# Performance work log

Measured on AMD Instinct MI355X. Metric: run time of the kernel, lower is better.

The kernel has to match this reference:

```python
import jax, jax.numpy as jnp
import numpy as np

EMBED_DIM = 200
INPUT_DIM = 512


def setup_inputs() -> dict:
    key = jax.random.key(0)
    k1, k2, k3, k4 = jax.random.split(key, 4)
    B, L, T = 64, 256, 64
    x = jax.random.normal(k1, (B, L, INPUT_DIM), dtype=jnp.float32)
    y = jax.random.normal(k2, (B, T, INPUT_DIM), dtype=jnp.float32)
    # fc = nn.Linear(input_dim, embedding_dim)
    W = jax.random.normal(k3, (EMBED_DIM, INPUT_DIM), dtype=jnp.float32) * (1.0 / np.sqrt(INPUT_DIM))
    b = jax.random.normal(k4, (EMBED_DIM,), dtype=jnp.float32) * 0.01
    return {"x": x, "y": y, "W": W, "b": b}


def reference(x, y, W, b):
    # Project both modalities (last dim != embedding_dim in original triggers fc)
    xp = jnp.einsum('bld,ed->ble', x, W) + b   # B x L x E
    yp = jnp.einsum('btd,ed->bte', y, W) + b   # B x T x E
    # Pairwise matchmap: for pair (i, j), matchmap = xp[i] @ yp[j].T -> L x T
    mm = jnp.einsum('ile,jte->ijlt', xp, yp)   # B x B x L x T
    # MISA: max over L (rows of matchmap, dim 0), then mean over T
    S = jnp.max(mm, axis=2).mean(axis=2)       # B x B
    return S
```

## Files before the change

kernel.cpp:

```cpp
#include <hip/hip_runtime.h>
#include <hip/hip_bf16.h>
#include <stdint.h>

#define BB 64
#define LL 256
#define TT 64
#define DD 512
#define EE 200
#define EP 208
#define NKK 13
#define NROWS_X 16384
#define BSTRIDE 264
#define PBM 80

typedef __attribute__((ext_vector_type(8))) short short8;
typedef __attribute__((ext_vector_type(4))) float floatx4;
typedef __attribute__((ext_vector_type(16))) float floatx16;

__device__ __forceinline__ short f2bf(float f) {
  uint32_t u = __builtin_bit_cast(uint32_t, f);
  u = (u + 0x7fffu + ((u >> 16) & 1u)) >> 16;
  return (short)u;
}

__device__ __forceinline__ uint32_t pack2(float lo, float hi) {
  return __builtin_amdgcn_perm(__builtin_bit_cast(uint32_t, hi),
                               __builtin_bit_cast(uint32_t, lo), 0x07060302u);
}

typedef const __attribute__((address_space(1))) uint32_t gu32_t;
typedef __attribute__((address_space(3))) uint32_t lu32_t;
__device__ __forceinline__ void glds16(const void* g, void* l) {
  __builtin_amdgcn_global_load_lds((gu32_t*)g, (lu32_t*)l, 16, 0, 0);
}

#define VMCNT_BARRIER(N) asm volatile("s_waitcnt vmcnt(" #N ") lgkmcnt(0)\n\ts_barrier" ::: "memory")

__global__ void wcvt_kernel(const float* __restrict__ W, short* __restrict__ Wb) {
  const int t = blockIdx.x * 256 + threadIdx.x;
  const int base = t * 8;
  const int e = base >> 9;
  short8 o;
  if (e < EE) {
    const floatx4 f0 = *(const floatx4*)(W + base);
    const floatx4 f1 = *(const floatx4*)(W + base + 4);
    o[0] = f2bf(f0.x); o[1] = f2bf(f0.y); o[2] = f2bf(f0.z); o[3] = f2bf(f0.w);
    o[4] = f2bf(f1.x); o[5] = f2bf(f1.y); o[6] = f2bf(f1.z); o[7] = f2bf(f1.w);
  } else {
    o = (short8)0;
  }
  *(short8*)(Wb + base) = o;
}

__global__ __launch_bounds__(320, 1) void proj_kernel(const float* __restrict__ x,
                                                      const float* __restrict__ y,
                                                      const short* __restrict__ Wb,
                                                      const float* __restrict__ bias,
                                                      short* __restrict__ pT) {
  __shared__ __align__(16) char smem[71680];
  float* ldsA = (float*)smem;
  short* ldsB = (short*)(smem + 30720);
  short* bounce = (short*)smem;

  const int tid  = threadIdx.x;
  const int lane = tid & 63;
  const int wid  = tid >> 6;
  const int r16   = lane & 15;
  const int khalf = lane >> 4;

  const int row0 = blockIdx.x * PBM;

  floatx4 acc[NKK];
#pragma unroll
  for (int n = 0; n < NKK; n++) acc[n] = (floatx4){0.f, 0.f, 0.f, 0.f};

  auto stage = [&](int buf, int ks) {
#pragma unroll
    for (int it = 0; it < 2; it++) {
      const int p = it * 320 + tid;
      const int r = p >> 3, c = p & 7;
      const int gr = row0 + r;
      const float* src = (gr < NROWS_X) ? (x + (size_t)gr * DD)
                                        : (y + (size_t)(gr - NROWS_X) * DD);
      glds16(src + ks * 32 + ((c ^ (r & 7)) << 2),
             &ldsA[buf * 2560 + p * 4]);
    }
#pragma unroll
    for (int it = 0; it < 3; it++) {
      const int p = it * 320 + tid;
      if (it < 2 || tid < 192) {
        const int r = p >> 2, c = p & 3;
        glds16(Wb + (size_t)r * DD + ks * 32 + ((c ^ ((r >> 1) & 3)) << 3),
               &ldsB[buf * 6656 + p * 8]);
      }
    }
  };

  auto compute = [&](int s) {
    const int buf = s % 3;
    const int r = wid * 16 + r16;
    const int c0 = (2 * khalf) ^ (r & 7);
    const int c1 = (2 * khalf + 1) ^ (r & 7);
    const floatx4 f0 = *(const floatx4*)&ldsA[buf * 2560 + r * 32 + c0 * 4];
    const floatx4 f1 = *(const floatx4*)&ldsA[buf * 2560 + r * 32 + c1 * 4];
    union { short8 s8; uint32_t u[4]; } af;
    af.u[0] = pack2(f0.x, f0.y);
    af.u[1] = pack2(f0.z, f0.w);
    af.u[2] = pack2(f1.x, f1.y);
    af.u[3] = pack2(f1.z, f1.w);
    const int bcol = (khalf ^ ((r16 >> 1) & 3)) << 3;
#pragma unroll
    for (int n = 0; n < NKK; n++) {
      const int erow = n * 16 + r16;
      const short8 bfrag = *(const short8*)&ldsB[buf * 6656 + erow * 32 + bcol];
      acc[n] = __builtin_amdgcn_mfma_f32_16x16x32_bf16(af.s8, bfrag, acc[n], 0, 0, 0);
    }
  };

  stage(0, 0);
  stage(1, 1);

  for (int s = 0; s < 15; s++) {
    VMCNT_BARRIER(4);
    if (s + 2 < 16) stage((s + 2) % 3, s + 2);
    compute(s);
  }
  VMCNT_BARRIER(0);
  compute(15);

  __syncthreads();

#pragma unroll
  for (int n = 0; n < NKK; n++) {
    const int e = n * 16 + r16;
    const float bv = (e < EE) ? bias[e] : 0.0f;
#pragma unroll
    for (int rr = 0; rr < 4; rr++) {
      const int lr = wid * 16 + khalf * 4 + rr;
      bounce[lr * BSTRIDE + e] = f2bf(acc[n][rr] + bv);
    }
  }
  __syncthreads();

  for (int c = tid; c < 2080; c += 320) {
    const int n    = c / 160;
    const int rem  = c - n * 160;
    const int lrow = rem >> 1;
    const int eh   = rem & 1;
    const int gr   = row0 + lrow;
    const short8 piece = *(const short8*)&bounce[lrow * BSTRIDE + n * 16 + eh * 8];
    *(short8*)&pT[((size_t)((gr >> 5) * 13 + n)) * 512 + (size_t)(((eh << 5) | (gr & 31)) * 8)] = piece;
  }
}

__global__ __launch_bounds__(512, 2) void pair_kernel(const short* __restrict__ xpT,
                                                      const short* __restrict__ ypT,
                                                      float* __restrict__ S) {
  __shared__ __align__(16) char lds[2 * 53248 + 16384];
  float* red = (float*)(lds + 2 * 53248);

  const int tid  = threadIdx.x;
  const int lane = tid & 63;
  const int wid  = tid >> 6;
  const int jj2  = wid >> 2;
  const int wj   = wid & 3;
  const int bid  = blockIdx.x;
  const int i    = bid & 63;
  const int jq   = bid >> 6;
  const int jbase = jq * 16;

  short8 a0[NKK], a1[NKK];
  {
    const short* ab0 = xpT + ((size_t)((i * 8 + wj * 2 + 0) * NKK)) * 512 + lane * 8;
    const short* ab1 = xpT + ((size_t)((i * 8 + wj * 2 + 1) * NKK)) * 512 + lane * 8;
#pragma unroll
    for (int kk = 0; kk < NKK; kk++) {
      a0[kk] = *(const short8*)(ab0 + kk * 512);
      a1[kk] = *(const short8*)(ab1 + kk * 512);
    }
  }

  auto stageB = [&](int g) {
    const short* src = ypT + (size_t)(jbase + g * 2) * 26 * 512;
    char* dst = lds + (g & 1) * 53248;
    for (int c = tid; c < 3328; c += 512)
      glds16(src + (size_t)c * 8, dst + c * 16);
  };

  stageB(0);
  __syncthreads();

  for (int g = 0; g < 8; g++) {
    if (g + 1 < 8) stageB(g + 1);

    const int j = g * 2 + jj2;
    const short* bbase = (const short*)(lds + (g & 1) * 53248) +
                         (size_t)(jj2 * 26 * 512) + lane * 8;

    floatx16 accA0n0, accA0n1, accA1n0, accA1n1;
#pragma unroll
    for (int r = 0; r < 16; r++) {
      accA0n0[r] = 0.f; accA0n1[r] = 0.f; accA1n0[r] = 0.f; accA1n1[r] = 0.f;
    }

#pragma unroll
    for (int kk = 0; kk < NKK; kk++) {
      const short8 b0 = *(const short8*)(bbase + (0 * NKK + kk) * 512);
      const short8 b1 = *(const short8*)(bbase + (1 * NKK + kk) * 512);
      accA0n0 = __builtin_amdgcn_mfma_f32_32x32x16_bf16(a0[kk], b0, accA0n0, 0, 0, 0);
      accA1n0 = __builtin_amdgcn_mfma_f32_32x32x16_bf16(a1[kk], b0, accA1n0, 0, 0, 0);
      accA0n1 = __builtin_amdgcn_mfma_f32_32x32x16_bf16(a0[kk], b1, accA0n1, 0, 0, 0);
      accA1n1 = __builtin_amdgcn_mfma_f32_32x32x16_bf16(a1[kk], b1, accA1n1, 0, 0, 0);
    }

    float v0 = accA0n0[0], v1 = accA0n1[0];
#pragma unroll
    for (int r = 0; r < 16; r++) {
      v0 = fmaxf(v0, accA0n0[r]); v0 = fmaxf(v0, accA1n0[r]);
      v1 = fmaxf(v1, accA0n1[r]); v1 = fmaxf(v1, accA1n1[r]);
    }
    v0 = fmaxf(v0, __shfl_xor(v0, 32, 64));
    v1 = fmaxf(v1, __shfl_xor(v1, 32, 64));
    if (lane < 32) {
      red[(j * 4 + wj) * 64 + 0 * 32 + lane] = v0;
      red[(j * 4 + wj) * 64 + 1 * 32 + lane] = v1;
    }

    __syncthreads();
  }

#pragma unroll
  for (int rep = 0; rep < 2; rep++) {
    const int j = wid * 2 + rep;
    const int t = lane;
    float v = red[(j * 4 + 0) * 64 + t];
    v = fmaxf(v, red[(j * 4 + 1) * 64 + t]);
    v = fmaxf(v, red[(j * 4 + 2) * 64 + t]);
    v = fmaxf(v, red[(j * 4 + 3) * 64 + t]);
    v += __shfl_xor(v, 1, 64);
    v += __shfl_xor(v, 2, 64);
    v += __shfl_xor(v, 4, 64);
    v += __shfl_xor(v, 8, 64);
    v += __shfl_xor(v, 16, 64);
    v += __shfl_xor(v, 32, 64);
    if (t == 0) S[i * BB + jbase + j] = v * (1.0f / 64.0f);
  }
}

extern "C" void kernel_launch(void* const* d_in, const int* in_sizes, int n_in,
                              void* d_out, int out_size, void* d_ws, size_t ws_size,
                              hipStream_t stream) {
  const float* x = (const float*)d_in[0];
  const float* y = (const float*)d_in[1];
  const float* W = (const float*)d_in[2];
  const float* b = (const float*)d_in[3];
  float* S = (float*)d_out;

  char* ws = (char*)d_ws;
  short* Wb = (short*)ws;
  short* pT = (short*)(ws + 262144);
  short* ypT = pT + (size_t)6656 * 512;

  wcvt_kernel<<<52, 256, 0, stream>>>(W, Wb);
  proj_kernel<<<256, 320, 0, stream>>>(x, y, Wb, b, pT);
  pair_kernel<<<256, 512, 0, stream>>>(pT, ypT, S);
}
```

Before: 45.43 us.

## Split projection N dimension across three wave groups with 960-thread blocks

The projection kernel grows from 5 to 15 waves per block. Each group of 5 waves covers the 16-row M tiles, but only about a third of the 13 E-column tiles (5/4/4), which cuts each wave's accumulator registers and serial MFMA chain. Staging loads are spread over more threads, so each thread issues two async loads instead of five, and the vmcnt wait is adjusted to match. This adds per-wave parallelism inside each CU at the cost of duplicate A-fragment conversion across the three groups, plus a divergent ncnt guard.

```diff
diff --git a/kernel.cpp b/kernel.cpp
--- a/kernel.cpp
+++ b/kernel.cpp
@@ -52,12 +52,12 @@
   *(short8*)(Wb + base) = o;
 }
 
-__global__ __launch_bounds__(320, 1) void proj_kernel(const float* __restrict__ x,
+__global__ __launch_bounds__(960, 1) void proj_kernel(const float* __restrict__ x,
                                                       const float* __restrict__ y,
                                                       const short* __restrict__ Wb,
                                                       const float* __restrict__ bias,
                                                       short* __restrict__ pT) {
-  __shared__ __align__(16) char smem[71680];
+  __shared__ __align__(16) char smem[70656];
   float* ldsA = (float*)smem;
   short* ldsB = (short*)(smem + 30720);
   short* bounce = (short*)smem;
@@ -67,38 +67,45 @@
   const int wid  = tid >> 6;
   const int r16   = lane & 15;
   const int khalf = lane >> 4;
+  const int mw = wid % 5;
+  const int eh = wid / 5;
+  const int nbase = (eh == 0) ? 0 : (eh == 1) ? 5 : 9;
+  const int ncnt  = (eh == 0) ? 5 : 4;
 
   const int row0 = blockIdx.x * PBM;
 
-  floatx4 acc[NKK];
-#pragma unroll
-  for (int n = 0; n < NKK; n++) acc[n] = (floatx4){0.f, 0.f, 0.f, 0.f};
+  floatx4 acc[5];
+#pragma unroll
+  for (int n = 0; n < 5; n++) acc[n] = (floatx4){0.f, 0.f, 0.f, 0.f};
 
   auto stage = [&](int buf, int ks) {
-#pragma unroll
-    for (int it = 0; it < 2; it++) {
-      const int p = it * 320 + tid;
-      const int r = p >> 3, c = p & 7;
-      const int gr = row0 + r;
-      const float* src = (gr < NROWS_X) ? (x + (size_t)gr * DD)
-                                        : (y + (size_t)(gr - NROWS_X) * DD);
-      glds16(src + ks * 32 + ((c ^ (r & 7)) << 2),
-             &ldsA[buf * 2560 + p * 4]);
-    }
-#pragma unroll
-    for (int it = 0; it < 3; it++) {
-      const int p = it * 320 + tid;
-      if (it < 2 || tid < 192) {
-        const int r = p >> 2, c = p & 3;
+    {
+      if (tid < 640) {
+        const int a = tid;
+        const int r = a >> 3, c = a & 7;
+        const int gr = row0 + r;
+        const float* src = (gr < NROWS_X) ? (x + (size_t)gr * DD)
+                                          : (y + (size_t)(gr - NROWS_X) * DD);
+        glds16(src + ks * 32 + ((c ^ (r & 7)) << 2),
+               &ldsA[buf * 2560 + a * 4]);
+      } else {
+        const int q = tid - 640;
+        const int r = q >> 2, c = q & 3;
         glds16(Wb + (size_t)r * DD + ks * 32 + ((c ^ ((r >> 1) & 3)) << 3),
-               &ldsB[buf * 6656 + p * 8]);
+               &ldsB[buf * 6656 + q * 8]);
       }
+    }
+    {
+      const int q = (tid < 512) ? (tid + 320) : (tid - 512);
+      const int r = q >> 2, c = q & 3;
+      glds16(Wb + (size_t)r * DD + ks * 32 + ((c ^ ((r >> 1) & 3)) << 3),
+             &ldsB[buf * 6656 + q * 8]);
     }
   };
 
   auto compute = [&](int s) {
     const int buf = s % 3;
-    const int r = wid * 16 + r16;
+    const int r = mw * 16 + r16;
     const int c0 = (2 * khalf) ^ (r & 7);
     const int c1 = (2 * khalf + 1) ^ (r & 7);
     const floatx4 f0 = *(const floatx4*)&ldsA[buf * 2560 + r * 32 + c0 * 4];
@@ -110,10 +117,12 @@
     af.u[3] = pack2(f1.z, f1.w);
     const int bcol = (khalf ^ ((r16 >> 1) & 3)) << 3;
 #pragma unroll
-    for (int n = 0; n < NKK; n++) {
-      const int erow = n * 16 + r16;
-      const short8 bfrag = *(const short8*)&ldsB[buf * 6656 + erow * 32 + bcol];
-      acc[n] = __builtin_amdgcn_mfma_f32_16x16x32_bf16(af.s8, bfrag, acc[n], 0, 0, 0);
+    for (int n = 0; n < 5; n++) {
+      if (n < ncnt) {
+        const int erow = (nbase + n) * 16 + r16;
+        const short8 bfrag = *(const short8*)&ldsB[buf * 6656 + erow * 32 + bcol];
+        acc[n] = __builtin_amdgcn_mfma_f32_16x16x32_bf16(af.s8, bfrag, acc[n], 0, 0, 0);
+      }
     }
   };
 
@@ -121,7 +130,7 @@
   stage(1, 1);
 
   for (int s = 0; s < 15; s++) {
-    VMCNT_BARRIER(4);
+    VMCNT_BARRIER(2);
     if (s + 2 < 16) stage((s + 2) % 3, s + 2);
     compute(s);
   }
@@ -130,26 +139,25 @@
 
   __syncthreads();
 
-#pragma unroll
-  for (int n = 0; n < NKK; n++) {
-    const int e = n * 16 + r16;
+  for (int n = 0; n < ncnt; n++) {
+    const int e = (nbase + n) * 16 + r16;
     const float bv = (e < EE) ? bias[e] : 0.0f;
 #pragma unroll
     for (int rr = 0; rr < 4; rr++) {
-      const int lr = wid * 16 + khalf * 4 + rr;
+      const int lr = mw * 16 + khalf * 4 + rr;
       bounce[lr * BSTRIDE + e] = f2bf(acc[n][rr] + bv);
     }
   }
   __syncthreads();
 
-  for (int c = tid; c < 2080; c += 320) {
+  for (int c = tid; c < 2080; c += 960) {
     const int n    = c / 160;
     const int rem  = c - n * 160;
     const int lrow = rem >> 1;
-    const int eh   = rem & 1;
+    const int ehh  = rem & 1;
     const int gr   = row0 + lrow;
-    const short8 piece = *(const short8*)&bounce[lrow * BSTRIDE + n * 16 + eh * 8];
-    *(short8*)&pT[((size_t)((gr >> 5) * 13 + n)) * 512 + (size_t)(((eh << 5) | (gr & 31)) * 8)] = piece;
+    const short8 piece = *(const short8*)&bounce[lrow * BSTRIDE + n * 16 + ehh * 8];
+    *(short8*)&pT[((size_t)((gr >> 5) * 13 + n)) * 512 + (size_t)(((ehh << 5) | (gr & 31)) * 8)] = piece;
   }
 }
 
@@ -262,6 +270,6 @@
   short* ypT = pT + (size_t)6656 * 512;
 
   wcvt_kernel<<<52, 256, 0, stream>>>(W, Wb);
-  proj_kernel<<<256, 320, 0, stream>>>(x, y, Wb, b, pT);
+  proj_kernel<<<256, 960, 0, stream>>>(x, y, Wb, b, pT);
   pair_kernel<<<256, 512, 0, stream>>>(pT, ypT, S);
 }
```

Result: no change. 44.96 us (-1.0%).
